# Performance work log

Measured on AMD Instinct MI355X. Metric: run time of the kernel, lower is better.

The kernel has to match this reference:

```python
import jax, jax.numpy as jnp
import numpy as np

B, N, F_IN, K, OUT = 64, 512, 6, 8, 3
SLOPE = 0.01  # torch LeakyReLU default negative_slope


def lrelu(x):
    return jnp.where(x >= 0, x, SLOPE * x)


def edge_mlp(e, w1, b1, w2, b2):
    # Linear -> LeakyReLU -> Linear -> LeakyReLU (EdgeConvMLP / mlp1)
    return lrelu(lrelu(e @ w1 + b1) @ w2 + b2)


def dyn_edge_conv(x, w1, b1, w2, b2):
    # x: [B, N, F]. kNN in feature space within each graph (self included,
    # matching torch_cluster.knn used by PyG DynamicEdgeConv).
    x2 = jnp.sum(x * x, -1)                                   # [B, N]
    d = x2[:, :, None] + x2[:, None, :] - 2.0 * jnp.einsum('bnf,bmf->bnm', x, x)
    idx = jax.lax.top_k(-d, K)[1]                              # [B, N, K]
    xj = jax.vmap(lambda xb, ib: xb[ib])(x, idx)               # [B, N, K, F]
    xi = jnp.broadcast_to(x[:, :, None, :], xj.shape)
    e = jnp.concatenate([xi, xj - xi], -1)                     # [B, N, K, 2F]
    h = edge_mlp(e, w1, b1, w2, b2)                            # [B, N, K, 256]
    return h.max(axis=2)                                       # max aggregation


def _lin(key, din, dout):
    kw, kb = jax.random.split(key)
    s = 1.0 / np.sqrt(din)
    w = jax.random.uniform(kw, (din, dout), jnp.float32, -s, s)
    b = jax.random.uniform(kb, (dout,), jnp.float32, -s, s)
    return w, b


def setup_inputs() -> dict:
    key = jax.random.key(0)
    ks = jax.random.split(key, 20)
    inp = {}
    inp['x'] = jax.random.normal(ks[0], (B * N, F_IN), jnp.float32)
    inp['edge_index'] = jax.random.randint(ks[1], (2, B * N * K), 0, B * N, jnp.int64)  # unused
    inp['batch'] = jnp.repeat(jnp.arange(B, dtype=jnp.int64), N)
    dims = [(2 * F_IN, 336, 256), (512, 336, 256), (512, 336, 256), (512, 336, 256)]
    for i, (din, dh, do) in enumerate(dims):
        w1, b1 = _lin(ks[2 + 2 * i], din, dh)
        w2, b2 = _lin(ks[3 + 2 * i], dh, do)
        inp[f'c{i+1}_w1'], inp[f'c{i+1}_b1'] = w1, b1
        inp[f'c{i+1}_w2'], inp[f'c{i+1}_b2'] = w2, b2
    inp['m1_w1'], inp['m1_b1'] = _lin(ks[10], 256 * 4 + F_IN, 336)
    inp['m1_w2'], inp['m1_b2'] = _lin(ks[11], 336, 256)
    inp['m2_w1'], inp['m2_b1'] = _lin(ks[12], 256, 128)
    inp['m2_w2'], inp['m2_b2'] = _lin(ks[13], 128, OUT)
    return inp


def reference(x, edge_index, batch,
              c1_w1, c1_b1, c1_w2, c1_b2,
              c2_w1, c2_b1, c2_w2, c2_b2,
              c3_w1, c3_b1, c3_w2, c3_b2,
              c4_w1, c4_b1, c4_w2, c4_b2,
              m1_w1, m1_b1, m1_w2, m1_b2,
              m2_w1, m2_b1, m2_w2, m2_b2):
    # edge_index is unused: DynamicEdgeConv rebuilds the kNN graph each layer.
    # Equal-sized graphs: reshape instead of segment ops (batch = repeat(arange(B), N)).
    xb = x.reshape(B, N, F_IN)
    x1 = dyn_edge_conv(xb, c1_w1, c1_b1, c1_w2, c1_b2)
    x2 = dyn_edge_conv(x1, c2_w1, c2_b1, c2_w2, c2_b2)
    x3 = dyn_edge_conv(x2, c3_w1, c3_b1, c3_w2, c3_b2)
    x4 = dyn_edge_conv(x3, c4_w1, c4_b1, c4_w2, c4_b2)
    h = jnp.concatenate([xb, x1, x2, x3, x4], -1)   # [B, N, 1030]
    h = edge_mlp(h, m1_w1, m1_b1, m1_w2, m1_b2)     # [B, N, 256]
    g = h.mean(axis=1)                              # global_mean_pool -> [B, 256]
    return lrelu(g @ m2_w1 + m2_b1) @ m2_w2 + m2_b2  # [B, OUT]
```

## Files before the change

### kernel.cpp

```cpp
#include <hip/hip_runtime.h>
#include <hip/hip_bf16.h>


#define DEVFN __device__ __forceinline__
DEVFN float lrelu(float v) { return v >= 0.f ? v : 0.01f * v; }

using bf16x8 = __attribute__((ext_vector_type(8))) short;
using f32x4  = __attribute__((ext_vector_type(4))) float;

template<int N> struct IC { static constexpr int value = N; };

DEVFN unsigned short f2bf(float v) {
    __hip_bfloat16 h = __float2bfloat16(v);
    return *(unsigned short*)&h;
}
DEVFN float bf2f(unsigned short u) {
    return __uint_as_float((unsigned)u << 16);
}

struct PDesc { const float* src; unsigned short* dst; int Kt, NT, N, mode, p0, p1, Ksrc; };
struct PTable { PDesc d[13]; };

__global__ __launch_bounds__(256) void pack_kernel(PTable tb) {
    PDesc d = tb.d[blockIdx.y];
    int i = blockIdx.x * 256 + threadIdx.x;
    int tot = d.Kt * d.NT * 512;
    if (i >= tot) return;
    int j = i & 7, lane = (i >> 3) & 63;
    int tile = i >> 9;
    int nt = tile % d.NT, kt = tile / d.NT;
    int k = kt * 32 + ((lane >> 4) << 3) + j;
    int n = nt * 16 + (lane & 15);
    float v = 0.f;
    if (d.mode == 0) {
        if (k < d.Ksrc) v = d.src[(size_t)k * d.N + n];
    } else if (d.mode == 1) {
        if (k < d.p1) v = d.src[(size_t)k * d.N + n] - d.src[(size_t)(k + d.p1) * d.N + n];
        else if (k >= d.p0 && k < d.p0 + d.p1) v = d.src[(size_t)(k - d.p0 + d.p1) * d.N + n];
    } else if (d.mode == 2) {
        if (k < 6) v = d.src[(size_t)k * d.N + n];
        else if (k >= 32 && k < 1056) v = d.src[(size_t)(k - 26) * d.N + n];
    } else {
        v = d.src[(size_t)(k + d.p0) * d.N + n];
    }
    d.dst[i] = f2bf(v);
}

__global__ __launch_bounds__(256) void xbprep_kernel(const float* __restrict__ xb,
                                                     unsigned short* __restrict__ xcat) {
    int p = blockIdx.x * 256 + threadIdx.x;
    if (p >= 32768) return;
    unsigned short r[16];
    #pragma unroll
    for (int c = 0; c < 6; ++c) r[c] = f2bf(xb[p * 6 + c]);
    #pragma unroll
    for (int c = 6; c < 16; ++c) r[c] = 0;
    unsigned short* xc = xcat + (size_t)p * 1056;
    #pragma unroll
    for (int c = 0; c < 16; ++c) xc[c] = r[c];
    #pragma unroll
    for (int c = 16; c < 32; ++c) xc[c] = 0;
}

template<int F>
__global__ __launch_bounds__(256) void norms_kernel(const float* __restrict__ f,
                                                    float* __restrict__ nrm) {
    int p = blockIdx.x * 256 + threadIdx.x;
    if (p >= 64 * 512) return;
    const float* r = f + (size_t)p * F;
    float s = 0.f;
    #pragma unroll
    for (int i = 0; i < F; ++i) s += r[i] * r[i];
    nrm[p] = s;
}

template<int F>
__global__ __launch_bounds__(256) void knn_kernel(const float* __restrict__ feat,
                                                  const float* __restrict__ nrm,
                                                  int* __restrict__ knn) {
    constexpr int FP = (F == 6) ? 8 : (F + 4);
    __shared__ float Xq[32 * FP];
    __shared__ float Xc[32 * FP];
    __shared__ float qn[32], cn[32];
    __shared__ float dt[32 * 33];
    const int t  = threadIdx.x;
    const int b  = blockIdx.x >> 4;
    const int n0 = (blockIdx.x & 15) << 5;
    const float* fg = feat + (size_t)b * 512 * F;

    for (int i = t; i < 32 * F; i += 256) {
        int r = i / F, c = i - r * F;
        Xq[r * FP + c] = fg[(size_t)(n0 + r) * F + c];
    }
    if (t < 32) qn[t] = nrm[b * 512 + n0 + t];

    float d8[8]; int i8[8];
    #pragma unroll
    for (int k = 0; k < 8; ++k) { d8[k] = 3.4e38f; i8[k] = 0; }

    const int q = t >> 3, cs = t & 7;

    for (int ct = 0; ct < 16; ++ct) {
        const int c0 = ct << 5;
        __syncthreads();
        for (int i = t; i < 32 * F; i += 256) {
            int r = i / F, c = i - r * F;
            Xc[r * FP + c] = fg[(size_t)(c0 + r) * F + c];
        }
        if (t < 32) cn[t] = nrm[b * 512 + c0 + t];
        __syncthreads();

        float acc[4] = {0.f, 0.f, 0.f, 0.f};
        #pragma unroll
        for (int f = 0; f < F; ++f) {
            float qv = Xq[q * FP + f];
            #pragma unroll
            for (int j = 0; j < 4; ++j) acc[j] += qv * Xc[(cs + 8 * j) * FP + f];
        }
        #pragma unroll
        for (int j = 0; j < 4; ++j)
            dt[q * 33 + cs + 8 * j] = qn[q] + cn[cs + 8 * j] - 2.f * acc[j];
        __syncthreads();

        if (t < 32) {
            #pragma unroll 1
            for (int i = 0; i < 32; ++i) {
                float d = dt[t * 33 + i];
                if (d < d8[7]) {
                    d8[7] = d; i8[7] = c0 + i;
                    #pragma unroll
                    for (int s = 7; s >= 1; --s) {
                        if (d8[s] < d8[s - 1]) {
                            float td = d8[s]; d8[s] = d8[s - 1]; d8[s - 1] = td;
                            int   ti = i8[s]; i8[s] = i8[s - 1]; i8[s - 1] = ti;
                        }
                    }
                }
            }
        }
    }
    if (t < 32) {
        #pragma unroll
        for (int k = 0; k < 8; ++k)
            knn[((size_t)b * 512 + n0 + t) * 8 + k] = i8[k];
    }
}

__global__ __launch_bounds__(256, 2)
void knn_mfma(const unsigned short* __restrict__ xfl,
              const float* __restrict__ nrm,
              int* __restrict__ knn) {
    __shared__ unsigned short Qh[64 * 72], Ql[64 * 72], Ch[64 * 72], Cl[64 * 72];
    __shared__ float dt[64 * 66];
    __shared__ float qn[64], cn[64];
    float* mD = dt;
    int*   mI = (int*)(dt + 2048);

    const int t  = threadIdx.x;
    const int l  = t & 63, w = t >> 6;
    const int m16 = l & 15, q4 = l >> 4;
    const int bx = blockIdx.x;
    const int slot = bx >> 3;
    const int b  = (bx & 7) + 8 * (slot >> 3);
    const int qs = (slot & 7) << 6;

    if (t < 64) qn[t] = nrm[b * 512 + qs + t];

    float d8[8]; int i8[8];
    #pragma unroll
    for (int k = 0; k < 8; ++k) { d8[k] = 3.4e38f; i8[k] = 0x7fffffff; }

    const int sr = t >> 2;
    const int sc = (t & 3) << 4;
    const int tq = t & 63, sub = t >> 6;

    for (int cs = 0; cs < 8; ++cs) {
        const int c0 = cs << 6;
        if (t < 64) cn[t] = nrm[b * 512 + c0 + t];

        f32x4 acc[4];
        #pragma unroll
        for (int i = 0; i < 4; ++i) acc[i] = (f32x4){0.f, 0.f, 0.f, 0.f};

        for (int kc = 0; kc < 4; ++kc) {
            const int k0 = kc << 6;
            __syncthreads();
            {
                const unsigned short* qr = xfl + (size_t)(b * 512 + qs + sr) * 512;
                const unsigned short* cr = xfl + (size_t)(b * 512 + c0 + sr) * 512;
                *(uint4*)&Qh[sr * 72 + sc]     = *(const uint4*)(qr + k0 + sc);
                *(uint4*)&Qh[sr * 72 + sc + 8] = *(const uint4*)(qr + k0 + sc + 8);
                *(uint4*)&Ql[sr * 72 + sc]     = *(const uint4*)(qr + 256 + k0 + sc);
                *(uint4*)&Ql[sr * 72 + sc + 8] = *(const uint4*)(qr + 256 + k0 + sc + 8);
                *(uint4*)&Ch[sr * 72 + sc]     = *(const uint4*)(cr + k0 + sc);
                *(uint4*)&Ch[sr * 72 + sc + 8] = *(const uint4*)(cr + k0 + sc + 8);
                *(uint4*)&Cl[sr * 72 + sc]     = *(const uint4*)(cr + 256 + k0 + sc);
                *(uint4*)&Cl[sr * 72 + sc + 8] = *(const uint4*)(cr + 256 + k0 + sc + 8);
            }
            __syncthreads();

            #pragma unroll
            for (int kt = 0; kt < 2; ++kt) {
                const int ko = kt * 32 + q4 * 8;
                bf16x8 ah = *(const bf16x8*)&Qh[(w * 16 + m16) * 72 + ko];
                bf16x8 al = *(const bf16x8*)&Ql[(w * 16 + m16) * 72 + ko];
                #pragma unroll
                for (int nt = 0; nt < 4; ++nt) {
                    bf16x8 bh = *(const bf16x8*)&Ch[(nt * 16 + m16) * 72 + ko];
                    bf16x8 bl = *(const bf16x8*)&Cl[(nt * 16 + m16) * 72 + ko];
                    acc[nt] = __builtin_amdgcn_mfma_f32_16x16x32_bf16(ah, bh, acc[nt], 0, 0, 0);
                    acc[nt] = __builtin_amdgcn_mfma_f32_16x16x32_bf16(ah, bl, acc[nt], 0, 0, 0);
                    acc[nt] = __builtin_amdgcn_mfma_f32_16x16x32_bf16(al, bh, acc[nt], 0, 0, 0);
                }
            }
        }

        #pragma unroll
        for (int nt = 0; nt < 4; ++nt) {
            float cv = cn[nt * 16 + m16];
            #pragma unroll
            for (int rr = 0; rr < 4; ++rr) {
                int qr = w * 16 + q4 * 4 + rr;
                dt[qr * 66 + nt * 16 + m16] = qn[qr] + cv - 2.f * acc[nt][rr];
            }
        }
        __syncthreads();

        {
            const float* drow = &dt[tq * 66 + sub * 16];
            #pragma unroll 1
            for (int j = 0; j < 16; ++j) {
                float d = drow[j];
                if (d < d8[7]) {
                    d8[7] = d; i8[7] = c0 + sub * 16 + j;
                    #pragma unroll
                    for (int s = 7; s >= 1; --s) {
                        if (d8[s] < d8[s - 1]) {
                            float td = d8[s]; d8[s] = d8[s - 1]; d8[s - 1] = td;
                            int   ti = i8[s]; i8[s] = i8[s - 1]; i8[s - 1] = ti;
                        }
                    }
                }
            }
        }
        __syncthreads();
    }

    #pragma unroll
    for (int k = 0; k < 8; ++k) {
        mD[(tq * 4 + sub) * 8 + k] = d8[k];
        mI[(tq * 4 + sub) * 8 + k] = i8[k];
    }
    __syncthreads();
    if (t < 64) {
        int p[4] = {0, 0, 0, 0};
        int outb = (b * 512 + qs + t) * 8;
        #pragma unroll 1
        for (int k = 0; k < 8; ++k) {
            float bd = 3.5e38f; int bi = 0x7fffffff; int bs = 0;
            #pragma unroll
            for (int s = 0; s < 4; ++s) {
                if (p[s] < 8) {
                    float dd = mD[(t * 4 + s) * 8 + p[s]];
                    int   ii = mI[(t * 4 + s) * 8 + p[s]];
                    if (dd < bd || (dd == bd && ii < bi)) { bd = dd; bi = ii; bs = s; }
                }
            }
            knn[outb + k] = bi;
            p[bs]++;
        }
    }
}

__global__ __launch_bounds__(256)
void pgemm1_kernel(const float* __restrict__ xb,
                   const float* __restrict__ W1,
                   const float* __restrict__ B1,
                   unsigned short* __restrict__ Pa,
                   unsigned short* __restrict__ Pb) {
    int i = blockIdx.x * 256 + threadIdx.x;
    if (i >= 32768 * 42) return;
    int p = i / 42, c8 = i - p * 42;
    int c0 = c8 * 8;
    float x[6];
    #pragma unroll
    for (int k = 0; k < 6; ++k) x[k] = xb[p * 6 + k];
    float sa[8], sb[8];
    #pragma unroll
    for (int j = 0; j < 8; ++j) { sa[j] = B1[c0 + j]; sb[j] = 0.f; }
    #pragma unroll
    for (int k = 0; k < 6; ++k) {
        const float* wra = W1 + (size_t)k * 336 + c0;
        const float* wrb = W1 + (size_t)(k + 6) * 336 + c0;
        #pragma unroll
        for (int j = 0; j < 8; ++j) {
            float wb = wrb[j];
            sa[j] += x[k] * (wra[j] - wb);
            sb[j] += x[k] * wb;
        }
    }
    unsigned short oa[8], ob[8];
    #pragma unroll
    for (int j = 0; j < 8; ++j) { oa[j] = f2bf(sa[j]); ob[j] = f2bf(sb[j]); }
    *(uint4*)&Pa[(size_t)p * 336 + c0] = *(uint4*)oa;
    *(uint4*)&Pb[(size_t)p * 336 + c0] = *(uint4*)ob;
}

__global__ __launch_bounds__(256, 2)
void pgemm_kernel(const unsigned short* __restrict__ xfl,
                  const unsigned short* __restrict__ Wa,
                  const unsigned short* __restrict__ Wb,
                  const float* __restrict__ B1,
                  unsigned short* __restrict__ Pa,
                  unsigned short* __restrict__ Pb) {
    __shared__ unsigned short smem[64 * 344];
    const int t = threadIdx.x;
    const int l = t & 63, w = t >> 6;
    const int q4 = l >> 4, m16 = l & 15;
    const int s1 = w * 6;
    const int bx = blockIdx.x & 511;
    const bool isA = !(blockIdx.x & 512);
    const unsigned short* W1ap = isA ? Wa : Wb;
    unsigned short*       Pp   = isA ? Pa : Pb;
    const int slot = bx >> 3;
    const int r0 = ((bx & 7) + 8 * (slot >> 3)) * 512 + (slot & 7) * 64;

    {
        const int r = t >> 2;
        const unsigned short* srow = xfl + (size_t)(r0 + r) * 512;
        #pragma unroll
        for (int s = 0; s < 8; ++s) {
            int c16 = (t & 3) + (s << 2);
            *(uint4*)&smem[r * 264 + c16 * 8] = *(const uint4*)(srow + c16 * 8);
        }
    }
    __syncthreads();

    f32x4 acc[4][6];
    #pragma unroll
    for (int mt = 0; mt < 4; ++mt)
        #pragma unroll
        for (int n = 0; n < 6; ++n) acc[mt][n] = (f32x4){0.f, 0.f, 0.f, 0.f};

    auto run = [&](auto c1c) {
        constexpr int C1 = decltype(c1c)::value;
        bf16x8 bcur[C1];
        {
            const unsigned short* bp = W1ap + ((size_t)s1 * 64 + l) * 8;
            #pragma unroll
            for (int n = 0; n < C1; ++n) bcur[n] = *(const bf16x8*)(bp + n * 512);
        }
        #pragma unroll 1
        for (int kt = 0; kt < 8; ++kt) {
            bf16x8 bnext[C1];
            if (kt + 1 < 8) {
                const unsigned short* bp = W1ap + ((size_t)((kt + 1) * 21 + s1) * 64 + l) * 8;
                #pragma unroll
                for (int n = 0; n < C1; ++n) bnext[n] = *(const bf16x8*)(bp + n * 512);
            }
            bf16x8 af[4];
            #pragma unroll
            for (int mt = 0; mt < 4; ++mt)
                af[mt] = *(const bf16x8*)&smem[(mt * 16 + m16) * 264 + q4 * 8 + kt * 32];
            #pragma unroll
            for (int n = 0; n < C1; ++n)
                #pragma unroll
                for (int mt = 0; mt < 4; ++mt)
                    acc[mt][n] = __builtin_amdgcn_mfma_f32_16x16x32_bf16(af[mt], bcur[n], acc[mt][n], 0, 0, 0);
            #pragma unroll
            for (int n = 0; n < C1; ++n) bcur[n] = bnext[n];
        }
    };
    if (w < 3) run(IC<6>{});
    else       run(IC<3>{});

    __syncthreads();
    {
        const int c1 = (w < 3) ? 6 : 3;
        for (int n = 0; n < c1; ++n) {
            int col = (s1 + n) * 16 + m16;
            float bias = isA ? B1[col] : 0.f;
            #pragma unroll
            for (int mt = 0; mt < 4; ++mt)
                #pragma unroll
                for (int r = 0; r < 4; ++r)
                    smem[(mt * 16 + q4 * 4 + r) * 344 + col] = f2bf(acc[mt][n][r] + bias);
        }
    }
    __syncthreads();
    {
        uint4* dst = (uint4*)(Pp + (size_t)r0 * 336);
        const uint4* src = (const uint4*)smem;
        #pragma unroll 1
        for (int i = t; i < 2688; i += 256)
            dst[i] = src[(i / 42) * 43 + (i % 42)];
    }
}

template<int MODE>
__global__ __launch_bounds__(256, MODE == 3 ? 4 : 3)
void mfma_mlp(const unsigned short* __restrict__ featbf,
              const int* __restrict__ knn,
              const unsigned short* __restrict__ W1p, const float* __restrict__ B1,
              const unsigned short* __restrict__ W2p, const float* __restrict__ B2,
              const unsigned short* __restrict__ Pp,
              const unsigned short* __restrict__ Pbp,
              float* __restrict__ outf,
              unsigned short* __restrict__ xcat, int sliceoff,
              unsigned short* __restrict__ xfl, float* __restrict__ nrm) {
    constexpr int ROWS = 32;

    __shared__ unsigned short smem[ROWS * 360];
    __shared__ int rowi[32];
    __shared__ int rowj[32];
    __shared__ float nparts[4][4];

    const int t = threadIdx.x;
    const int l = t & 63, w = t >> 6;
    const int q4 = l >> 4, m16 = l & 15;
    const int s1 = w * 6;
    const int s2 = w * 4;

    const int bx = blockIdx.x;
    int p0;
    if constexpr (MODE == 3) {
        int slot = bx >> 3;
        int g = (bx & 7) + 8 * (slot >> 7);
        p0 = g * 512 + (slot & 127) * 4;
    } else {
        int slot = bx >> 3;
        int g = (bx & 7) + 8 * (slot >> 4);
        p0 = g * 512 + (slot & 15) * 32;
    }

    if constexpr (MODE == 3) {
        if (t < 32) {
            int pt = p0 + (t >> 3);
            rowi[t] = pt;
            rowj[t] = (pt & ~511) + knn[pt * 8 + (t & 7)];
        }
        __syncthreads();
        const int row = t >> 3;
        const int u0  = t & 7;
        const unsigned short* va = Pp  + (size_t)rowi[row] * 336;
        const unsigned short* vb = Pbp + (size_t)rowj[row] * 336;
        uint4 A[6], Bv[6];
        #pragma unroll
        for (int k = 0; k < 6; ++k) {
            int u = u0 + 8 * k;
            if (u < 42) {
                A[k]  = *(const uint4*)(va + u * 8);
                Bv[k] = *(const uint4*)(vb + u * 8);
            }
        }
        #pragma unroll
        for (int k = 0; k < 6; ++k) {
            int u = u0 + 8 * k;
            if (u < 42) {
                const unsigned short* sa = (const unsigned short*)&A[k];
                const unsigned short* sb = (const unsigned short*)&Bv[k];
                uint4 ov;
                unsigned short* o = (unsigned short*)&ov;
                #pragma unroll
                for (int j = 0; j < 8; ++j)
                    o[j] = f2bf(lrelu(bf2f(sa[j]) + bf2f(sb[j])));
                *(uint4*)&smem[row * 360 + u * 8] = ov;
            }
        }
    } else {
        f32x4 acc1[2][6];
        #pragma unroll
        for (int mt = 0; mt < 2; ++mt)
            #pragma unroll
            for (int n = 0; n < 6; ++n) acc1[mt][n] = (f32x4){0.f, 0.f, 0.f, 0.f};

        auto g1 = [&](auto c1c, int ktbase) {
            constexpr int C1 = decltype(c1c)::value;
            bf16x8 bcur[C1];
            {
                const unsigned short* bp =
                    W1p + ((size_t)(ktbase * 21 + s1) * 64 + l) * 8;
                #pragma unroll
                for (int n = 0; n < C1; ++n) bcur[n] = *(const bf16x8*)(bp + n * 512);
            }
            #pragma unroll 1
            for (int kt = 0; kt < 11; ++kt) {
                bf16x8 bnext[C1];
                if (kt + 1 < 11) {
                    const unsigned short* bp =
                        W1p + ((size_t)((ktbase + kt + 1) * 21 + s1) * 64 + l) * 8;
                    #pragma unroll
                    for (int n = 0; n < C1; ++n) bnext[n] = *(const bf16x8*)(bp + n * 512);
                }
                bf16x8 af[2];
                #pragma unroll
                for (int mt = 0; mt < 2; ++mt)
                    af[mt] = *(const bf16x8*)&smem[(mt * 16 + m16) * 360 + q4 * 8 + kt * 32];
                #pragma unroll
                for (int n = 0; n < C1; ++n)
                    #pragma unroll
                    for (int mt = 0; mt < 2; ++mt)
                        acc1[mt][n] = __builtin_amdgcn_mfma_f32_16x16x32_bf16(af[mt], bcur[n], acc1[mt][n], 0, 0, 0);
                #pragma unroll
                for (int n = 0; n < C1; ++n) bcur[n] = bnext[n];
            }
        };

        for (int kc = 0; kc < 3; ++kc) {
            __syncthreads();
            {
                const int r = t >> 3, tc = t & 7;
                const unsigned short* srow =
                    featbf + (size_t)(p0 + r) * 1056 + kc * 352;
                #pragma unroll
                for (int s = 0; s < 6; ++s) {
                    int c16 = tc + (s << 3);
                    if (c16 < 44)
                        *(uint4*)&smem[r * 360 + c16 * 8] = *(const uint4*)(srow + c16 * 8);
                }
            }
            __syncthreads();

            if (w < 3) g1(IC<6>{}, kc * 11);
            else       g1(IC<3>{}, kc * 11);
        }
        __syncthreads();

        {
            const int c1 = (w < 3) ? 6 : 3;
            for (int n = 0; n < c1; ++n) {
                int nt = s1 + n;
                float b = B1[nt * 16 + m16];
                #pragma unroll
                for (int mt = 0; mt < 2; ++mt) {
                    #pragma unroll
                    for (int r = 0; r < 4; ++r) {
                        int row = mt * 16 + q4 * 4 + r;
                        float v = acc1[mt][n][r] + b;
                        smem[row * 360 + nt * 16 + m16] = f2bf(lrelu(v));
                    }
                }
            }
        }
    }

    if (t < ROWS) {
        #pragma unroll
        for (int c = 336; c < 352; ++c) smem[t * 360 + c] = 0;
    }
    __syncthreads();

    f32x4 acc2[2][4];
    #pragma unroll
    for (int mt = 0; mt < 2; ++mt)
        #pragma unroll
        for (int n = 0; n < 4; ++n) acc2[mt][n] = (f32x4){0.f, 0.f, 0.f, 0.f};
    {
        bf16x8 b0[4], b1f[4];
        {
            const unsigned short* bp0 = W2p + ((size_t)s2 * 64 + l) * 8;
            const unsigned short* bp1 = W2p + ((size_t)(16 + s2) * 64 + l) * 8;
            #pragma unroll
            for (int n = 0; n < 4; ++n) {
                b0[n]  = *(const bf16x8*)(bp0 + n * 512);
                b1f[n] = *(const bf16x8*)(bp1 + n * 512);
            }
        }
        #pragma unroll 1
        for (int kt = 0; kt < 11; ++kt) {
            bf16x8 b2[4];
            if (kt + 2 < 11) {
                const unsigned short* bp = W2p + ((size_t)((kt + 2) * 16 + s2) * 64 + l) * 8;
                #pragma unroll
                for (int n = 0; n < 4; ++n) b2[n] = *(const bf16x8*)(bp + n * 512);
            }
            bf16x8 af[2];
            #pragma unroll
            for (int mt = 0; mt < 2; ++mt)
                af[mt] = *(const bf16x8*)&smem[(mt * 16 + m16) * 360 + q4 * 8 + kt * 32];
            #pragma unroll
            for (int n = 0; n < 4; ++n)
                #pragma unroll
                for (int mt = 0; mt < 2; ++mt)
                    acc2[mt][n] = __builtin_amdgcn_mfma_f32_16x16x32_bf16(af[mt], b0[n], acc2[mt][n], 0, 0, 0);
            #pragma unroll
            for (int n = 0; n < 4; ++n) { b0[n] = b1f[n]; b1f[n] = b2[n]; }
        }
    }

    if constexpr (MODE == 3) {
        __syncthreads();
        unsigned short* sh = smem;
        #pragma unroll
        for (int mt = 0; mt < 2; ++mt) {
            float nsum = 0.f;
            int plocal = mt * 2 + (q4 >> 1);
            #pragma unroll
            for (int n = 0; n < 4; ++n) {
                int nt = s2 + n;
                float b = B2[nt * 16 + m16];
                float mv = -3.4e38f;
                #pragma unroll
                for (int r = 0; r < 4; ++r) mv = fmaxf(mv, lrelu(acc2[mt][n][r] + b));
                mv = fmaxf(mv, __shfl_xor(mv, 16, 64));
                if ((q4 & 1) == 0) {
                    int col = nt * 16 + m16;
                    unsigned short hi = f2bf(mv);
                    float fhi = bf2f(hi);
                    unsigned short lo = f2bf(mv - fhi);
                    float xr = fhi + bf2f(lo);
                    nsum += xr * xr;
                    sh[plocal * 512 + col] = hi;
                    sh[plocal * 512 + 256 + col] = lo;
                }
            }
            #pragma unroll
            for (int o = 1; o < 16; o <<= 1) nsum += __shfl_xor(nsum, o, 64);
            if ((q4 & 1) == 0 && m16 == 0) nparts[plocal][w] = nsum;
        }
        __syncthreads();
        {
            int r = t >> 6, cb = (t & 63) * 8;
            int p = p0 + r;
            uint4 v0 = *(uint4*)&sh[r * 512 + cb];
            *(uint4*)&xfl[(size_t)p * 512 + cb] = v0;
            if (cb < 256)
                *(uint4*)&xcat[(size_t)p * 1056 + sliceoff + cb] = v0;
        }
        if (t < 4)
            nrm[p0 + t] =
                nparts[t][0] + nparts[t][1] + nparts[t][2] + nparts[t][3];
    } else {
        #pragma unroll
        for (int mt = 0; mt < 2; ++mt)
            #pragma unroll
            for (int n = 0; n < 4; ++n) {
                int nt = s2 + n;
                float b = B2[nt * 16 + m16];
                int col = nt * 16 + m16;
                #pragma unroll
                for (int r = 0; r < 4; ++r) {
                    int p = p0 + mt * 16 + q4 * 4 + r;
                    outf[(size_t)p * 256 + col] = lrelu(acc2[mt][n][r] + b);
                }
            }
    }
}

__global__ __launch_bounds__(256) void pool_kernel(const float* __restrict__ h,
                                                   float* __restrict__ g) {
    int b = blockIdx.x, t = threadIdx.x;
    const float* hb = h + (size_t)b * 512 * 256;
    float s = 0.f;
    for (int n = 0; n < 512; ++n) s += hb[n * 256 + t];
    g[b * 256 + t] = s * (1.f / 512.f);
}

__global__ __launch_bounds__(128) void head_kernel(const float* __restrict__ g,
                                                   const float* __restrict__ w1,
                                                   const float* __restrict__ b1,
                                                   const float* __restrict__ w2,
                                                   const float* __restrict__ b2,
                                                   float* __restrict__ out) {
    __shared__ float gs[256];
    __shared__ float hid[128];
    int b = blockIdx.x, t = threadIdx.x;
    gs[t] = g[b * 256 + t];
    gs[t + 128] = g[b * 256 + t + 128];
    __syncthreads();
    float s = b1[t];
    for (int c = 0; c < 256; ++c) s += gs[c] * w1[c * 128 + t];
    hid[t] = lrelu(s);
    __syncthreads();
    if (t < 3) {
        float o = b2[t];
        for (int j = 0; j < 128; ++j) o += hid[j] * w2[j * 3 + t];
        out[b * 3 + t] = o;
    }
}

extern "C" void kernel_launch(void* const* d_in, const int* in_sizes, int n_in,
                              void* d_out, int out_size, void* d_ws, size_t ws_size,
                              hipStream_t stream) {
    const float* xb = (const float*)d_in[0];
    const float* c_w1[4] = { (const float*)d_in[3],  (const float*)d_in[7],
                             (const float*)d_in[11], (const float*)d_in[15] };
    const float* c_b1[4] = { (const float*)d_in[4],  (const float*)d_in[8],
                             (const float*)d_in[12], (const float*)d_in[16] };
    const float* c_w2[4] = { (const float*)d_in[5],  (const float*)d_in[9],
                             (const float*)d_in[13], (const float*)d_in[17] };
    const float* c_b2[4] = { (const float*)d_in[6],  (const float*)d_in[10],
                             (const float*)d_in[14], (const float*)d_in[18] };
    const float* m1w1 = (const float*)d_in[19];
    const float* m1b1 = (const float*)d_in[20];
    const float* m1w2 = (const float*)d_in[21];
    const float* m1b2 = (const float*)d_in[22];
    const float* m2w1 = (const float*)d_in[23];
    const float* m2b1 = (const float*)d_in[24];
    const float* m2w2 = (const float*)d_in[25];
    const float* m2b2 = (const float*)d_in[26];

    char* base = (char*)d_ws;
    size_t off = 0;
    auto alloc = [&](size_t bytes) { char* p = base + off; off = (off + bytes + 255) & ~(size_t)255; return p; };
    int*            knn   = (int*)           alloc((size_t)32768 * 8 * 4);
    float*          nrm   = (float*)         alloc((size_t)32768 * 4);
    char*           Preg  =                  alloc((size_t)32768 * 256 * 4);
    unsigned short* Ppb   = (unsigned short*)alloc((size_t)32768 * 336 * 2);
    float*          g     = (float*)         alloc(64 * 256 * 4);
    unsigned short* xcat  = (unsigned short*)alloc((size_t)32768 * 1056 * 2);
    unsigned short* xfl   = (unsigned short*)alloc((size_t)32768 * 512 * 2);
    unsigned short* w1p1  = (unsigned short*)alloc((size_t)1  * 21 * 512 * 2);
    unsigned short* w2p1  = (unsigned short*)alloc((size_t)11 * 16 * 512 * 2);
    unsigned short* w1a[3]; unsigned short* w1b[3]; unsigned short* w2p[3];
    for (int i = 0; i < 3; ++i) {
        w1a[i] = (unsigned short*)alloc((size_t)8  * 21 * 512 * 2);
        w1b[i] = (unsigned short*)alloc((size_t)8  * 21 * 512 * 2);
        w2p[i] = (unsigned short*)alloc((size_t)11 * 16 * 512 * 2);
    }
    unsigned short* m1p1  = (unsigned short*)alloc((size_t)33 * 21 * 512 * 2);
    unsigned short* m1p2  = (unsigned short*)alloc((size_t)11 * 16 * 512 * 2);
    unsigned short* Pp = (unsigned short*)Preg;
    float*          hm = (float*)Preg;

    PTable tb;
    tb.d[0] = { c_w1[0], w1p1, 1,  21, 336, 1, 16,  6,   0   };
    tb.d[1] = { c_w2[0], w2p1, 11, 16, 256, 0, 0,   0,   336 };
    for (int i = 0; i < 3; ++i) {
        tb.d[2 + 3 * i] = { c_w1[i + 1], w1a[i], 8,  21, 336, 1, 0,   256, 0   };
        tb.d[3 + 3 * i] = { c_w1[i + 1], w1b[i], 8,  21, 336, 3, 256, 0,   0   };
        tb.d[4 + 3 * i] = { c_w2[i + 1], w2p[i], 11, 16, 256, 0, 0,   0,   336 };
    }
    tb.d[11] = { m1w1, m1p1, 33, 21, 336, 2, 0, 0, 0   };
    tb.d[12] = { m1w2, m1p2, 11, 16, 256, 0, 0, 0, 336 };
    pack_kernel<<<dim3(1386, 13), dim3(256), 0, stream>>>(tb);
    xbprep_kernel<<<128, 256, 0, stream>>>(xb, xcat);

    norms_kernel<6><<<128, 256, 0, stream>>>(xb, nrm);
    knn_kernel<6><<<1024, 256, 0, stream>>>(xb, nrm, knn);
    pgemm1_kernel<<<5376, 256, 0, stream>>>(xb, c_w1[0], c_b1[0], Pp, Ppb);
    mfma_mlp<3><<<8192, 256, 0, stream>>>(nullptr, knn,
                                          nullptr, nullptr, w2p1, c_b2[0], Pp, Ppb,
                                          nullptr, xcat, 32, xfl, nrm);

    for (int l = 1; l < 4; ++l) {
        int dstslice = 32 + l * 256;
        knn_mfma<<<512, 256, 0, stream>>>(xfl, nrm, knn);
        pgemm_kernel<<<1024, 256, 0, stream>>>(xfl, w1a[l - 1], w1b[l - 1], c_b1[l], Pp, Ppb);
        mfma_mlp<3><<<8192, 256, 0, stream>>>(nullptr, knn,
                                              nullptr, nullptr, w2p[l - 1], c_b2[l], Pp, Ppb,
                                              nullptr, xcat, dstslice, xfl, nrm);
    }

    mfma_mlp<2><<<1024, 256, 0, stream>>>(xcat, nullptr,
                                          m1p1, m1b1, m1p2, m1b2, nullptr, nullptr,
                                          hm, nullptr, 0, nullptr, nullptr);

    pool_kernel<<<64, 256, 0, stream>>>(hm, g);
    head_kernel<<<64, 128, 0, stream>>>(g, m2w1, m2b1, m2w2, m2b2, (float*)d_out);
}
```

Baseline: 1.010 ms.

## Fuse mean pool into final MLP, keep kNN queries in registers, tweak occupancy

The final MLP epilogue now reduces LeakyReLU outputs across rows with shuffles and atomically adds the scaled sums into the pooled buffer. This removes the separate pool kernel and the full hidden-matrix write and read. The pooled buffer is zeroed inside the prep kernel. Separately, knn_mfma loads query fragments into registers once instead of restaging them through shared memory for every candidate tile, and pgemm's launch bounds now ask for 3 blocks per SM. The bf16 add-plus-LeakyReLU path is rewritten to unpack pairs from 32-bit words, and lrelu becomes fmaxf. Trade-offs are float atomics that make the summation order nondeterministic and higher register pressure in knn_mfma.

```diff
diff --git a/kernel.cpp b/kernel.cpp
--- a/kernel.cpp
+++ b/kernel.cpp
@@ -3,7 +3,7 @@
 
 
 #define DEVFN __device__ __forceinline__
-DEVFN float lrelu(float v) { return v >= 0.f ? v : 0.01f * v; }
+DEVFN float lrelu(float v) { return fmaxf(v, 0.01f * v); }
 
 using bf16x8 = __attribute__((ext_vector_type(8))) short;
 using f32x4  = __attribute__((ext_vector_type(4))) float;
@@ -47,9 +47,11 @@
 }
 
 __global__ __launch_bounds__(256) void xbprep_kernel(const float* __restrict__ xb,
-                                                     unsigned short* __restrict__ xcat) {
+                                                     unsigned short* __restrict__ xcat,
+                                                     float* __restrict__ g) {
     int p = blockIdx.x * 256 + threadIdx.x;
     if (p >= 32768) return;
+    if (p < 16384) g[p] = 0.f;
     unsigned short r[16];
     #pragma unroll
     for (int c = 0; c < 6; ++c) r[c] = f2bf(xb[p * 6 + c]);
@@ -150,7 +152,7 @@
 void knn_mfma(const unsigned short* __restrict__ xfl,
               const float* __restrict__ nrm,
               int* __restrict__ knn) {
-    __shared__ unsigned short Qh[64 * 72], Ql[64 * 72], Ch[64 * 72], Cl[64 * 72];
+    __shared__ unsigned short Ch[64 * 72], Cl[64 * 72];
     __shared__ float dt[64 * 66];
     __shared__ float qn[64], cn[64];
     float* mD = dt;
@@ -166,6 +168,18 @@
 
     if (t < 64) qn[t] = nrm[b * 512 + qs + t];
 
+    bf16x8 qh[4][2], ql[4][2];
+    {
+        const unsigned short* qr = xfl + (size_t)(b * 512 + qs + w * 16 + m16) * 512;
+        #pragma unroll
+        for (int kc = 0; kc < 4; ++kc)
+            #pragma unroll
+            for (int kt = 0; kt < 2; ++kt) {
+                qh[kc][kt] = *(const bf16x8*)(qr + kc * 64 + kt * 32 + q4 * 8);
+                ql[kc][kt] = *(const bf16x8*)(qr + 256 + kc * 64 + kt * 32 + q4 * 8);
+            }
+    }
+
     float d8[8]; int i8[8];
     #pragma unroll
     for (int k = 0; k < 8; ++k) { d8[k] = 3.4e38f; i8[k] = 0x7fffffff; }
@@ -182,16 +196,12 @@
         #pragma unroll
         for (int i = 0; i < 4; ++i) acc[i] = (f32x4){0.f, 0.f, 0.f, 0.f};
 
+        #pragma unroll
         for (int kc = 0; kc < 4; ++kc) {
             const int k0 = kc << 6;
             __syncthreads();
             {
-                const unsigned short* qr = xfl + (size_t)(b * 512 + qs + sr) * 512;
                 const unsigned short* cr = xfl + (size_t)(b * 512 + c0 + sr) * 512;
-                *(uint4*)&Qh[sr * 72 + sc]     = *(const uint4*)(qr + k0 + sc);
-                *(uint4*)&Qh[sr * 72 + sc + 8] = *(const uint4*)(qr + k0 + sc + 8);
-                *(uint4*)&Ql[sr * 72 + sc]     = *(const uint4*)(qr + 256 + k0 + sc);
-                *(uint4*)&Ql[sr * 72 + sc + 8] = *(const uint4*)(qr + 256 + k0 + sc + 8);
                 *(uint4*)&Ch[sr * 72 + sc]     = *(const uint4*)(cr + k0 + sc);
                 *(uint4*)&Ch[sr * 72 + sc + 8] = *(const uint4*)(cr + k0 + sc + 8);
                 *(uint4*)&Cl[sr * 72 + sc]     = *(const uint4*)(cr + 256 + k0 + sc);
@@ -202,8 +212,8 @@
             #pragma unroll
             for (int kt = 0; kt < 2; ++kt) {
                 const int ko = kt * 32 + q4 * 8;
-                bf16x8 ah = *(const bf16x8*)&Qh[(w * 16 + m16) * 72 + ko];
-                bf16x8 al = *(const bf16x8*)&Ql[(w * 16 + m16) * 72 + ko];
+                bf16x8 ah = qh[kc][kt];
+                bf16x8 al = ql[kc][kt];
                 #pragma unroll
                 for (int nt = 0; nt < 4; ++nt) {
                     bf16x8 bh = *(const bf16x8*)&Ch[(nt * 16 + m16) * 72 + ko];
@@ -306,7 +316,7 @@
     *(uint4*)&Pb[(size_t)p * 336 + c0] = *(uint4*)ob;
 }
 
-__global__ __launch_bounds__(256, 2)
+__global__ __launch_bounds__(256, 3)
 void pgemm_kernel(const unsigned short* __restrict__ xfl,
                   const unsigned short* __restrict__ Wa,
                   const unsigned short* __restrict__ Wb,
@@ -457,13 +467,18 @@
         for (int k = 0; k < 6; ++k) {
             int u = u0 + 8 * k;
             if (u < 42) {
-                const unsigned short* sa = (const unsigned short*)&A[k];
-                const unsigned short* sb = (const unsigned short*)&Bv[k];
+                const unsigned* ua = (const unsigned*)&A[k];
+                const unsigned* ub = (const unsigned*)&Bv[k];
                 uint4 ov;
                 unsigned short* o = (unsigned short*)&ov;
                 #pragma unroll
-                for (int j = 0; j < 8; ++j)
-                    o[j] = f2bf(lrelu(bf2f(sa[j]) + bf2f(sb[j])));
+                for (int j = 0; j < 4; ++j) {
+                    unsigned va_ = ua[j], vb_ = ub[j];
+                    float slo = __uint_as_float(va_ << 16) + __uint_as_float(vb_ << 16);
+                    float shi = __uint_as_float(va_ & 0xffff0000u) + __uint_as_float(vb_ & 0xffff0000u);
+                    o[2 * j]     = f2bf(lrelu(slo));
+                    o[2 * j + 1] = f2bf(lrelu(shi));
+                }
                 *(uint4*)&smem[row * 360 + u * 8] = ov;
             }
         }
@@ -631,29 +646,23 @@
             nrm[p0 + t] =
                 nparts[t][0] + nparts[t][1] + nparts[t][2] + nparts[t][3];
     } else {
-        #pragma unroll
-        for (int mt = 0; mt < 2; ++mt)
-            #pragma unroll
-            for (int n = 0; n < 4; ++n) {
-                int nt = s2 + n;
-                float b = B2[nt * 16 + m16];
-                int col = nt * 16 + m16;
-                #pragma unroll
-                for (int r = 0; r < 4; ++r) {
-                    int p = p0 + mt * 16 + q4 * 4 + r;
-                    outf[(size_t)p * 256 + col] = lrelu(acc2[mt][n][r] + b);
-                }
-            }
-    }
-}
-
-__global__ __launch_bounds__(256) void pool_kernel(const float* __restrict__ h,
-                                                   float* __restrict__ g) {
-    int b = blockIdx.x, t = threadIdx.x;
-    const float* hb = h + (size_t)b * 512 * 256;
-    float s = 0.f;
-    for (int n = 0; n < 512; ++n) s += hb[n * 256 + t];
-    g[b * 256 + t] = s * (1.f / 512.f);
+        const int bgraph = p0 >> 9;
+        #pragma unroll
+        for (int n = 0; n < 4; ++n) {
+            int nt = s2 + n;
+            float b = B2[nt * 16 + m16];
+            float s = 0.f;
+            #pragma unroll
+            for (int mt = 0; mt < 2; ++mt)
+                #pragma unroll
+                for (int r = 0; r < 4; ++r)
+                    s += lrelu(acc2[mt][n][r] + b);
+            s += __shfl_xor(s, 16, 64);
+            s += __shfl_xor(s, 32, 64);
+            if (q4 == 0)
+                atomicAdd(outf + bgraph * 256 + nt * 16 + m16, s * (1.f / 512.f));
+        }
+    }
 }
 
 __global__ __launch_bounds__(128) void head_kernel(const float* __restrict__ g,
@@ -721,7 +730,6 @@
     unsigned short* m1p1  = (unsigned short*)alloc((size_t)33 * 21 * 512 * 2);
     unsigned short* m1p2  = (unsigned short*)alloc((size_t)11 * 16 * 512 * 2);
     unsigned short* Pp = (unsigned short*)Preg;
-    float*          hm = (float*)Preg;
 
     PTable tb;
     tb.d[0] = { c_w1[0], w1p1, 1,  21, 336, 1, 16,  6,   0   };
@@ -734,7 +742,7 @@
     tb.d[11] = { m1w1, m1p1, 33, 21, 336, 2, 0, 0, 0   };
     tb.d[12] = { m1w2, m1p2, 11, 16, 256, 0, 0, 0, 336 };
     pack_kernel<<<dim3(1386, 13), dim3(256), 0, stream>>>(tb);
-    xbprep_kernel<<<128, 256, 0, stream>>>(xb, xcat);
+    xbprep_kernel<<<128, 256, 0, stream>>>(xb, xcat, g);
 
     norms_kernel<6><<<128, 256, 0, stream>>>(xb, nrm);
     knn_kernel<6><<<1024, 256, 0, stream>>>(xb, nrm, knn);
@@ -754,8 +762,7 @@
 
     mfma_mlp<2><<<1024, 256, 0, stream>>>(xcat, nullptr,
                                           m1p1, m1b1, m1p2, m1b2, nullptr, nullptr,
-                                          hm, nullptr, 0, nullptr, nullptr);
-
-    pool_kernel<<<64, 256, 0, stream>>>(hm, g);
+                                          g, nullptr, 0, nullptr, nullptr);
+
     head_kernel<<<64, 128, 0, stream>>>(g, m2w1, m2b1, m2w2, m2b2, (float*)d_out);
 }
```

Result: faster. 956.5 us (-5.3%).
